# Optimization experiments

Measured on AMD Instinct MI355X. Metric: run time of the kernel, lower is better.

Reference implementation:

```python
import jax, jax.numpy as jnp
import numpy as np

# Model dims
P_SPECS = [(6, 256), (7, 256)]          # pattern_length -> num_patterns (ordered)
P = 512                                  # total_num_patterns
MAXL = 7                                 # max_pattern_length
ND = 2                                   # num_diags (self-loop diag + main diag)
D = 300                                  # embedding_dim
V = 50000                                # vocab size
B = 32                                   # batch size
T = 128                                  # max_doc_len
NC = 2                                   # num_classes
NEG = -1e30                              # max-sum semiring zero; one = 0.0
END_STATES = np.concatenate([np.full(n, l - 1, dtype=np.int32) for l, n in P_SPECS])


def setup_inputs() -> dict:
    key = jax.random.key(0)
    ks = jax.random.split(key, 8)
    tokens = jax.random.randint(ks[0], (B, T), 0, V, dtype=jnp.int32)
    doc_lens = jax.random.randint(ks[1], (B,), 64, T + 1, dtype=jnp.int32)
    emb_table = jax.random.normal(ks[2], (V, D), dtype=jnp.float32)
    diags = jax.random.normal(ks[3], (P * ND * MAXL, D), dtype=jnp.float32)
    diags = diags / jnp.linalg.norm(diags, axis=1, keepdims=True)  # normalize(diags)
    bias = jax.random.normal(ks[4], (P * ND * MAXL, 1), dtype=jnp.float32)
    epsilons = jax.random.normal(ks[5], (P, MAXL - 1), dtype=jnp.float32)
    bn_weight = jnp.ones((P,), jnp.float32)
    bn_bias = jnp.zeros((P,), jnp.float32)
    final_w = 0.05 * jax.random.normal(ks[6], (NC, P), dtype=jnp.float32)
    final_b = jnp.zeros((NC,), jnp.float32)
    return dict(tokens=tokens, doc_lens=doc_lens, emb_table=emb_table, diags=diags,
                bias=bias, epsilons=epsilons, bn_weight=bn_weight, bn_bias=bn_bias,
                final_w=final_w, final_b=final_b)


def reference(tokens, doc_lens, emb_table, diags, bias, epsilons,
              bn_weight, bn_bias, final_w, final_b):
    # --- transition matrices (max-sum semiring: from_outer is identity) ---
    emb = emb_table[tokens]                                   # [B,T,D]
    # mm(diags, embeddings) + bias_scale * bias  (bias_scale = 1.0)
    ts = jnp.einsum('btd,kd->btk', emb, diags) + bias[:, 0]   # [B,T,P*ND*MAXL]
    ts = ts.reshape(B, T, P, ND, MAXL)                        # [B,T,P,ND,MAXL]

    end = jnp.asarray(END_STATES)                             # [P]
    hid0 = jnp.full((B, P, MAXL), NEG, jnp.float32).at[:, :, 0].set(0.0)
    sc0 = jnp.full((B, P), NEG, jnp.float32)                  # semiring.zero
    zpad = jnp.full((B, P, 1), NEG, jnp.float32)              # zero_padding
    rpad = jnp.zeros((B, P, 1), jnp.float32)                  # restart_padding (one)

    # epsilon_values = epsilon_scale (one=0) + epsilons
    def step(carry, xs):
        hid, sc = carry
        tm, i = xs                                            # tm: [B,P,ND,MAXL]
        # epsilon transitions
        ae = jnp.maximum(hid, jnp.concatenate([zpad, hid[:, :, :-1] + epsilons], axis=2))
        # main path: diag index -1 (the main diagonal)
        main = jnp.concatenate([rpad, ae[:, :, :-1] + tm[:, :, -1, :-1]], axis=2)
        # self loops: diag 0, self_loop_scale = semiring.one = 0
        sl = ae + tm[:, :, 0, :]
        hid = jnp.maximum(main, sl)
        endv = jnp.take_along_axis(hid, jnp.broadcast_to(end[None, :, None], (B, P, 1)), axis=2)[:, :, 0]
        sc = jnp.where((doc_lens > i)[:, None], jnp.maximum(sc, endv), sc)
        return (hid, sc), None

    (_, scores), _ = jax.lax.scan(step, (hid0, sc0),
                                  (jnp.moveaxis(ts, 1, 0), jnp.arange(T, dtype=jnp.int32)))

    # BatchNorm1d (training mode: biased batch statistics)
    mean = scores.mean(axis=0)
    var = scores.var(axis=0)
    scores = (scores - mean) * jax.lax.rsqrt(var + 1e-5) * bn_weight + bn_bias
    # binarize_scores
    scores = jnp.sign(jax.nn.relu(scores))
    # final linear layer
    return scores @ final_w.T + final_b                       # [B, NC]
```

## Files before the change

### kernel.cpp

```cpp
#include <hip/hip_runtime.h>

#define BB 32
#define TT 128
#define PP 512
#define DD 300
#define KT 10
#define NX 7168
#define AT 256
#define BT 448
#define NEG -1e30f

typedef _Float16 half8 __attribute__((ext_vector_type(8)));
typedef float floatx4 __attribute__((ext_vector_type(4)));

__device__ __forceinline__ floatx4 mfma16(half8 a, half8 b, floatx4 c) {
    return __builtin_amdgcn_mfma_f32_16x16x32_f16(a, b, c, 0, 0, 0);
}

__global__ __launch_bounds__(256) void pack_kernel(
    const int* __restrict__ tokens, const float* __restrict__ emb,
    const float* __restrict__ diags, const float* __restrict__ bias,
    _Float16* __restrict__ AhP, _Float16* __restrict__ AlP,
    _Float16* __restrict__ BhP, _Float16* __restrict__ BlP)
{
    const int idx = blockIdx.x * 256 + threadIdx.x;
    if (idx >= (AT + BT) * KT * 64) return;
    const int chunk = idx >> 6;
    const int ln = idx & 63;

    const float* src;
    float kslot;
    _Float16 *dh, *dl;
    int kt;
    if (chunk < AT * KT) {
        const int mt = chunk / KT; kt = chunk - mt * KT;
        const int m = mt * 16 + (ln & 15);
        src = emb + (size_t)tokens[m] * DD;
        kslot = 1.0f;
        dh = AhP + (size_t)chunk * 512 + ln * 8;
        dl = AlP + (size_t)chunk * 512 + ln * 8;
    } else {
        const int c2 = chunk - AT * KT;
        const int nt = c2 / KT; kt = c2 - nt * KT;
        const int n = nt * 16 + (ln & 15);
        src = diags + (size_t)n * DD;
        kslot = bias[n];
        dh = BhP + (size_t)c2 * 512 + ln * 8;
        dl = BlP + (size_t)c2 * 512 + ln * 8;
    }

    const int k0 = kt * 32 + (ln >> 4) * 8;
    float v[8];
    if (k0 + 8 <= DD) {
        float4 a = *(const float4*)(src + k0);
        float4 b = *(const float4*)(src + k0 + 4);
        v[0] = a.x; v[1] = a.y; v[2] = a.z; v[3] = a.w;
        v[4] = b.x; v[5] = b.y; v[6] = b.z; v[7] = b.w;
    } else {
        #pragma unroll
        for (int i = 0; i < 8; ++i) {
            const int k = k0 + i;
            v[i] = (k < DD) ? src[k] : (k == DD ? kslot : 0.f);
        }
    }
    half8 h, l;
    #pragma unroll
    for (int i = 0; i < 8; ++i) {
        h[i] = (_Float16)v[i];
        l[i] = (_Float16)((v[i] - (float)h[i]) * 4096.f);
    }
    *(half8*)dh = h;
    *(half8*)dl = l;
}

__global__ __launch_bounds__(256, 2) void gemm_kernel(
    const _Float16* __restrict__ AhP, const _Float16* __restrict__ AlP,
    const _Float16* __restrict__ BhP, const _Float16* __restrict__ BlP,
    const int* __restrict__ doc_lens,
    float* __restrict__ C)
{
    const int tid = threadIdx.x;
    const int w = tid >> 6, ln = tid & 63;
    const int n0t = blockIdx.x * 8, m0t = blockIdx.y * 8;
    const int wm = w & 1, wn = w >> 1;

    const int dl = doc_lens[blockIdx.y];

    floatx4 acc0[4][4], acc1[4][4];
    #pragma unroll
    for (int i = 0; i < 4; ++i)
        #pragma unroll
        for (int j = 0; j < 4; ++j) {
            acc0[i][j] = (floatx4){0.f, 0.f, 0.f, 0.f};
            acc1[i][j] = (floatx4){0.f, 0.f, 0.f, 0.f};
        }

    half8 ah[2][4], al[2][4];

    auto loadA = [&](int kt, int pb) {
        #pragma unroll
        for (int i = 0; i < 4; ++i) {
            const size_t ch = ((size_t)(m0t + wm * 4 + i) * KT + kt) * 512 + ln * 8;
            ah[pb][i] = *(const half8*)(AhP + ch);
            al[pb][i] = *(const half8*)(AlP + ch);
        }
    };

    loadA(0, 0);

    #pragma unroll
    for (int kt = 0; kt < KT; ++kt) {
        const int cb = kt & 1, nb = cb ^ 1;
        if (kt + 1 < KT) loadA(kt + 1, nb);
        #pragma unroll
        for (int j = 0; j < 4; ++j) {
            const size_t ch = ((size_t)(n0t + wn * 4 + j) * KT + kt) * 512 + ln * 8;
            const half8 bh = *(const half8*)(BhP + ch);
            const half8 bl = *(const half8*)(BlP + ch);
            #pragma unroll
            for (int i = 0; i < 4; ++i) {
                acc0[i][j] = mfma16(ah[cb][i], bh, acc0[i][j]);
                acc1[i][j] = mfma16(ah[cb][i], bl, acc1[i][j]);
                acc1[i][j] = mfma16(al[cb][i], bh, acc1[i][j]);
            }
        }
    }

    #pragma unroll
    for (int j = 0; j < 4; ++j) {
        const int n = (n0t + wn * 4 + j) * 16 + (ln & 15);
        #pragma unroll
        for (int i = 0; i < 4; ++i) {
            if ((wm * 4 + i) * 16 < dl) {
                const int mb = (m0t + wm * 4 + i) * 16 + (ln >> 4) * 4;
                #pragma unroll
                for (int r = 0; r < 4; ++r)
                    C[(size_t)(mb + r) * NX + n] =
                        acc0[i][j][r] + acc1[i][j][r] * (1.0f / 4096.0f);
            }
        }
    }
}

__global__ __launch_bounds__(64) void scan_kernel(
    const float* __restrict__ ts,
    const float* __restrict__ epsilons,
    const int* __restrict__ doc_lens,
    float* __restrict__ scores)
{
    const int b = blockIdx.x;
    const int p = blockIdx.y * 64 + threadIdx.x;
    const int dl = doc_lens[b];

    float e[6];
    #pragma unroll
    for (int i = 0; i < 6; ++i) e[i] = epsilons[p * 6 + i];

    const float* base = ts + (size_t)b * TT * NX + p * 14;

    float h0 = 0.f, h1 = NEG, h2 = NEG, h3 = NEG, h4 = NEG, h5 = NEG, h6 = NEG;
    float sc = NEG;
    const bool end5 = (p < 256);

    float2 buf[4][7];

    auto load = [&](int slot, int t) {
        const float2* s = (const float2*)(base + (size_t)t * NX);
        #pragma unroll
        for (int i = 0; i < 7; ++i) buf[slot][i] = s[i];
    };
    auto step = [&](int slot) {
        const float2* v = buf[slot];
        float ae0 = h0;
        float ae1 = fmaxf(h1, h0 + e[0]);
        float ae2 = fmaxf(h2, h1 + e[1]);
        float ae3 = fmaxf(h3, h2 + e[2]);
        float ae4 = fmaxf(h4, h3 + e[3]);
        float ae5 = fmaxf(h5, h4 + e[4]);
        float ae6 = fmaxf(h6, h5 + e[5]);
        h0 = fmaxf(0.f,            ae0 + v[0].x);
        h1 = fmaxf(ae0 + v[3].y,   ae1 + v[0].y);
        h2 = fmaxf(ae1 + v[4].x,   ae2 + v[1].x);
        h3 = fmaxf(ae2 + v[4].y,   ae3 + v[1].y);
        h4 = fmaxf(ae3 + v[5].x,   ae4 + v[2].x);
        h5 = fmaxf(ae4 + v[5].y,   ae5 + v[2].y);
        h6 = fmaxf(ae5 + v[6].x,   ae6 + v[3].x);
        sc = fmaxf(sc, end5 ? h5 : h6);
    };

    #pragma unroll
    for (int j = 0; j < 4; ++j) load(j, j);

    int tb = 0;
    for (; tb + 4 <= dl; tb += 4) {
        #pragma unroll
        for (int j = 0; j < 4; ++j) {
            step(j);
            const int t = tb + j + 4;
            load(j, t > 127 ? 127 : t);
        }
    }
    const int rem = dl - tb;
    #pragma unroll
    for (int j = 0; j < 3; ++j)
        if (j < rem) step(j);

    scores[p * BB + b] = sc;
}

__global__ __launch_bounds__(512) void finalize_kernel(
    const float* __restrict__ scores,
    const float* __restrict__ bn_w,
    const float* __restrict__ bn_b,
    const float* __restrict__ fw,
    const float* __restrict__ fb,
    float* __restrict__ out)
{
    __shared__ float acc[64];
    const int p = threadIdx.x;
    if (p < 64) acc[p] = 0.f;
    __syncthreads();

    float x[32];
    const float4* sp = (const float4*)(scores + p * 32);
    #pragma unroll
    for (int i = 0; i < 8; ++i) ((float4*)x)[i] = sp[i];

    float mean = 0.f;
    #pragma unroll
    for (int i = 0; i < 32; ++i) mean += x[i];
    mean *= (1.f / 32.f);
    float var = 0.f;
    #pragma unroll
    for (int i = 0; i < 32; ++i) { const float d = x[i] - mean; var = fmaf(d, d, var); }
    var *= (1.f / 32.f);

    const float scale = (1.f / sqrtf(var + 1e-5f)) * bn_w[p];
    const float shift = bn_b[p];
    const float w0 = fw[p], w1 = fw[PP + p];

    for (int b = 0; b < 32; ++b) {
        const float v = (x[b] - mean) * scale + shift;
        const bool bin = v > 0.f;
        float v0 = bin ? w0 : 0.f;
        float v1 = bin ? w1 : 0.f;
        #pragma unroll
        for (int o = 32; o; o >>= 1) {
            v0 += __shfl_xor(v0, o);
            v1 += __shfl_xor(v1, o);
        }
        if ((threadIdx.x & 63) == 0) {
            atomicAdd(&acc[b * 2 + 0], v0);
            atomicAdd(&acc[b * 2 + 1], v1);
        }
    }
    __syncthreads();
    if (p < 64) out[p] = acc[p] + fb[p & 1];
}

extern "C" void kernel_launch(void* const* d_in, const int* in_sizes, int n_in,
                              void* d_out, int out_size, void* d_ws, size_t ws_size,
                              hipStream_t stream) {
    const int*   tokens   = (const int*)d_in[0];
    const int*   doc_lens = (const int*)d_in[1];
    const float* emb      = (const float*)d_in[2];
    const float* diags    = (const float*)d_in[3];
    const float* bias     = (const float*)d_in[4];
    const float* eps      = (const float*)d_in[5];
    const float* bnw      = (const float*)d_in[6];
    const float* bnb      = (const float*)d_in[7];
    const float* fw       = (const float*)d_in[8];
    const float* fb       = (const float*)d_in[9];
    float* out = (float*)d_out;

    float* ts     = (float*)d_ws;
    float* scores = ts + (size_t)4096 * NX;
    _Float16* AhP = (_Float16*)(scores + PP * BB);
    _Float16* AlP = AhP + (size_t)AT * KT * 512;
    _Float16* BhP = AlP + (size_t)AT * KT * 512;
    _Float16* BlP = BhP + (size_t)BT * KT * 512;

    pack_kernel<<<(AT + BT) * KT * 64 / 256, 256, 0, stream>>>(
        tokens, emb, diags, bias, AhP, AlP, BhP, BlP);
    gemm_kernel<<<dim3(BT / 8, AT / 8), 256, 0, stream>>>(
        AhP, AlP, BhP, BlP, doc_lens, ts);
    scan_kernel<<<dim3(BB, PP / 64), 64, 0, stream>>>(ts, eps, doc_lens, scores);
    finalize_kernel<<<1, 512, 0, stream>>>(scores, bnw, bnb, fw, fb, out);
}
```

Baseline: 237.9 us.

## Stage B tiles in LDS via async global_load_lds with double buffering

```diff
diff --git a/kernel.cpp b/kernel.cpp
--- a/kernel.cpp
+++ b/kernel.cpp
@@ -12,6 +12,12 @@
 
 typedef _Float16 half8 __attribute__((ext_vector_type(8)));
 typedef float floatx4 __attribute__((ext_vector_type(4)));
+
+__device__ __forceinline__ void async_load16(const void* g, void* l) {
+    __builtin_amdgcn_global_load_lds(
+        (const __attribute__((address_space(1))) void*)g,
+        (__attribute__((address_space(3))) void*)l, 16, 0, 0);
+}
 
 __device__ __forceinline__ floatx4 mfma16(half8 a, half8 b, floatx4 c) {
     return __builtin_amdgcn_mfma_f32_16x16x32_f16(a, b, c, 0, 0, 0);
@@ -79,6 +85,8 @@
     const int* __restrict__ doc_lens,
     float* __restrict__ C)
 {
+    __shared__ __align__(16) _Float16 Bs[2][2][2][8][512];
+
     const int tid = threadIdx.x;
     const int w = tid >> 6, ln = tid & 63;
     const int n0t = blockIdx.x * 8, m0t = blockIdx.y * 8;
@@ -105,25 +113,44 @@
             al[pb][i] = *(const half8*)(AlP + ch);
         }
     };
-
+    auto stageB2 = [&](int kt0, int buf) {
+        #pragma unroll
+        for (int q = 0; q < 2; ++q)
+            #pragma unroll
+            for (int s = 0; s < 2; ++s) {
+                const int nt = w + s * 4;
+                const size_t ch = ((size_t)(n0t + nt) * KT + (kt0 + q)) * 512 + ln * 8;
+                async_load16(BhP + ch, &Bs[buf][q][0][nt][0]);
+                async_load16(BlP + ch, &Bs[buf][q][1][nt][0]);
+            }
+    };
+
+    stageB2(0, 0);
     loadA(0, 0);
-
-    #pragma unroll
-    for (int kt = 0; kt < KT; ++kt) {
-        const int cb = kt & 1, nb = cb ^ 1;
-        if (kt + 1 < KT) loadA(kt + 1, nb);
-        #pragma unroll
-        for (int j = 0; j < 4; ++j) {
-            const size_t ch = ((size_t)(n0t + wn * 4 + j) * KT + kt) * 512 + ln * 8;
-            const half8 bh = *(const half8*)(BhP + ch);
-            const half8 bl = *(const half8*)(BlP + ch);
+    __syncthreads();
+
+    #pragma unroll
+    for (int ph = 0; ph < 5; ++ph) {
+        const int cb = ph & 1, nb = cb ^ 1;
+        if (ph + 1 < 5) stageB2(2 * ph + 2, nb);
+        #pragma unroll
+        for (int q = 0; q < 2; ++q) {
+            const int kt = 2 * ph + q;
+            const int ab = kt & 1;
+            if (kt + 1 < KT) loadA(kt + 1, ab ^ 1);
             #pragma unroll
-            for (int i = 0; i < 4; ++i) {
-                acc0[i][j] = mfma16(ah[cb][i], bh, acc0[i][j]);
-                acc1[i][j] = mfma16(ah[cb][i], bl, acc1[i][j]);
-                acc1[i][j] = mfma16(al[cb][i], bh, acc1[i][j]);
+            for (int j = 0; j < 4; ++j) {
+                const half8 bh = *(const half8*)&Bs[cb][q][0][wn * 4 + j][ln * 8];
+                const half8 bl = *(const half8*)&Bs[cb][q][1][wn * 4 + j][ln * 8];
+                #pragma unroll
+                for (int i = 0; i < 4; ++i) {
+                    acc0[i][j] = mfma16(ah[ab][i], bh, acc0[i][j]);
+                    acc1[i][j] = mfma16(ah[ab][i], bl, acc1[i][j]);
+                    acc1[i][j] = mfma16(al[ab][i], bh, acc1[i][j]);
+                }
             }
         }
+        __syncthreads();
     }
 
     #pragma unroll
```

Result: faster. 202.3 us (-14.9%).
